# Optimization experiments

Hardware: AMD Instinct MI355X
Metric: run time of the kernel (lower is better)

Reference implementation:

```python
import jax, jax.numpy as jnp
import numpy as np

ALPHA = 1.0
BETA = 0.5

B, N, E = 4096, 4096, 16384


def setup_inputs() -> dict:
    key = jax.random.key(0)
    k1, k2, k3, k4, k5 = jax.random.split(key, 5)
    outputs = jax.random.normal(k1, (B, N), dtype=jnp.float32)
    targets = jax.random.uniform(k2, (B, N), dtype=jnp.float32)
    # per-node level weight (equivalent to node_levels dict -> level_weights lookup)
    level_w = jax.random.uniform(k3, (N,), dtype=jnp.float32)
    edge_src = jax.random.randint(k4, (E,), 0, N, dtype=jnp.int32)  # parent i
    edge_dst = jax.random.randint(k5, (E,), 0, N, dtype=jnp.int32)  # child  j
    return {"outputs": outputs, "targets": targets, "level_w": level_w,
            "edge_src": edge_src, "edge_dst": edge_dst}


def reference(outputs, targets, level_w, edge_src, edge_dst):
    # BCEWithLogits, reduction='none': softplus(x) - x*t (numerically stable)
    bce = jax.nn.softplus(outputs) - outputs * targets          # [B, N]
    weighted_bce = bce * level_w[None, :]                        # [B, N]

    probs = jax.nn.sigmoid(outputs)                              # [B, N]
    # for each edge (i=parent, j=child): consistency[:, j] += relu(p[:, j] - p[:, i])
    diff = jax.nn.relu(probs[:, edge_dst] - probs[:, edge_src])  # [B, E]
    consistency = jnp.zeros_like(probs).at[:, edge_dst].add(diff)  # [B, N]

    return ALPHA * weighted_bce.mean() + BETA * consistency.mean()
```

## Files before the change

kernel.cpp:

```cpp
#include <hip/hip_runtime.h>
#include <math.h>


#define ALPHA_C 1.0f
#define BETA_C  0.5f

constexpr int B = 4096;
constexpr int N = 4096;
constexpr int E = 16384;
constexpr int THREADS = 512;
constexpr int R = 4;

typedef _Float16 h4 __attribute__((ext_vector_type(4)));

__global__ __launch_bounds__(64) void init_out_kernel(float* out) {
    if (threadIdx.x == 0) out[0] = 0.0f;
}

__device__ __forceinline__ void fast_sig_sp(float x, float& p, float& sp) {
    float q = __expf(-fabsf(x));
    float d = 1.0f + q;
    float r = __builtin_amdgcn_rcpf(d);
    p  = (x >= 0.0f) ? r : q * r;
    sp = fmaxf(x, 0.0f) + __logf(d);
}

__global__ __launch_bounds__(THREADS, 8) void hier_loss_kernel(
    const float* __restrict__ outputs,
    const float* __restrict__ targets,
    const float* __restrict__ level_w,
    const int*   __restrict__ edge_src,
    const int*   __restrict__ edge_dst,
    float*       __restrict__ out)
{
    __shared__ h4 P[N];

    const int r0  = blockIdx.x * R;
    const int tid = threadIdx.x;

    const float4* out4 = (const float4*)outputs;
    const float4* tgt4 = (const float4*)targets;
    const float4* lw4  = (const float4*)level_w;

    float s1 = 0.0f;
#pragma unroll
    for (int j = 0; j < N / 4 / THREADS; ++j) {
        const int n4 = tid + j * THREADS;
        const float4 w = lw4[n4];
        const float wv[4] = {w.x, w.y, w.z, w.w};
        float4 xs[R], ts[R];
#pragma unroll
        for (int r = 0; r < R; ++r) {
            xs[r] = out4[(size_t)(r0 + r) * (N / 4) + n4];
            ts[r] = tgt4[(size_t)(r0 + r) * (N / 4) + n4];
        }
        h4 tmp[4];
#pragma unroll
        for (int r = 0; r < R; ++r) {
            const float xv[4] = {xs[r].x, xs[r].y, xs[r].z, xs[r].w};
            const float tv[4] = {ts[r].x, ts[r].y, ts[r].z, ts[r].w};
#pragma unroll
            for (int k = 0; k < 4; ++k) {
                float p, sp;
                fast_sig_sp(xv[k], p, sp);
                s1 = fmaf(wv[k], sp - xv[k] * tv[k], s1);
                tmp[k][r] = (_Float16)p;
            }
        }
#pragma unroll
        for (int k = 0; k < 4; ++k) P[4 * n4 + k] = tmp[k];
    }
    __syncthreads();

    h4 acc0 = {0, 0, 0, 0};
    h4 acc1 = {0, 0, 0, 0};
    const h4 zero = {0, 0, 0, 0};
    const int4* es4 = (const int4*)edge_src;
    const int4* ed4 = (const int4*)edge_dst;
#pragma unroll
    for (int j = 0; j < E / 4 / THREADS; ++j) {
        const int i = tid + j * THREADS;
        const int4 s = es4[i];
        const int4 d = ed4[i];
        h4 a0 = P[s.x], c0 = P[d.x];
        h4 a1 = P[s.y], c1 = P[d.y];
        h4 a2 = P[s.z], c2 = P[d.z];
        h4 a3 = P[s.w], c3 = P[d.w];
        acc0 += __builtin_elementwise_max(c0 - a0, zero);
        acc1 += __builtin_elementwise_max(c1 - a1, zero);
        acc0 += __builtin_elementwise_max(c2 - a2, zero);
        acc1 += __builtin_elementwise_max(c3 - a3, zero);
    }
    float s2 = 0.0f;
#pragma unroll
    for (int l = 0; l < 4; ++l) s2 += (float)acc0[l] + (float)acc1[l];

#pragma unroll
    for (int off = 32; off > 0; off >>= 1) {
        s1 += __shfl_down(s1, off, 64);
        s2 += __shfl_down(s2, off, 64);
    }
    __syncthreads();
    float* red = (float*)P;
    const int wave = tid >> 6;
    const int lane = tid & 63;
    if (lane == 0) { red[wave] = s1; red[8 + wave] = s2; }
    __syncthreads();
    if (tid == 0) {
        float a = 0.0f, c = 0.0f;
#pragma unroll
        for (int w = 0; w < 8; ++w) { a += red[w]; c += red[8 + w]; }
        const float inv = 1.0f / ((float)B * (float)N);
        atomicAdd(out, (ALPHA_C * a + BETA_C * c) * inv);
    }
}

extern "C" void kernel_launch(void* const* d_in, const int* in_sizes, int n_in,
                              void* d_out, int out_size, void* d_ws, size_t ws_size,
                              hipStream_t stream) {
    const float* outputs = (const float*)d_in[0];
    const float* targets = (const float*)d_in[1];
    const float* level_w = (const float*)d_in[2];
    const int*   edge_src = (const int*)d_in[3];
    const int*   edge_dst = (const int*)d_in[4];
    float* out = (float*)d_out;

    init_out_kernel<<<1, 64, 0, stream>>>(out);
    hier_loss_kernel<<<B / R, THREADS, 0, stream>>>(outputs, targets, level_w,
                                                    edge_src, edge_dst, out);
}
```

Baseline: 156.3 us.

## Make blocks persistent over row groups with double-buffered LDS and prefetch

The grid shrinks to 256 blocks of 1024 threads. Each block walks several 4-row groups and keeps its edge indices in registers, so they are loaded once per block rather than once per row group. Probabilities go into a double-buffered LDS array, and the next group's logits and targets are prefetched while the current group's edge gather runs. This cuts repeated edge-index traffic and overlaps global loads with the LDS gather phase. The cost is lower occupancy per CU and more register pressure.

Result: no change. 154.6 us, median of 2 (-1.1%).

```diff
diff --git a/kernel.cpp b/kernel.cpp
--- a/kernel.cpp
+++ b/kernel.cpp
@@ -8,8 +8,11 @@
 constexpr int B = 4096;
 constexpr int N = 4096;
 constexpr int E = 16384;
-constexpr int THREADS = 512;
+constexpr int THREADS = 1024;
 constexpr int R = 4;
+constexpr int GRID = 256;
+constexpr int GPB = (B / R) / GRID;
+constexpr int EJ = E / 4 / THREADS;
 
 typedef _Float16 h4 __attribute__((ext_vector_type(4)));
 
@@ -25,7 +28,7 @@
     sp = fmaxf(x, 0.0f) + __logf(d);
 }
 
-__global__ __launch_bounds__(THREADS, 8) void hier_loss_kernel(
+__global__ __launch_bounds__(THREADS, 4) void hier_loss_kernel(
     const float* __restrict__ outputs,
     const float* __restrict__ targets,
     const float* __restrict__ level_w,
@@ -33,27 +36,37 @@
     const int*   __restrict__ edge_dst,
     float*       __restrict__ out)
 {
-    __shared__ h4 P[N];
+    __shared__ h4 P[2][N];
 
-    const int r0  = blockIdx.x * R;
     const int tid = threadIdx.x;
+    const int g0  = blockIdx.x * GPB;
 
     const float4* out4 = (const float4*)outputs;
     const float4* tgt4 = (const float4*)targets;
     const float4* lw4  = (const float4*)level_w;
+    const int4*   es4  = (const int4*)edge_src;
+    const int4*   ed4  = (const int4*)edge_dst;
 
-    float s1 = 0.0f;
+    const float4 w = lw4[tid];
+    const float wv[4] = {w.x, w.y, w.z, w.w};
+
+    int4 se[EJ], de[EJ];
 #pragma unroll
-    for (int j = 0; j < N / 4 / THREADS; ++j) {
-        const int n4 = tid + j * THREADS;
-        const float4 w = lw4[n4];
-        const float wv[4] = {w.x, w.y, w.z, w.w};
-        float4 xs[R], ts[R];
+    for (int j = 0; j < EJ; ++j) {
+        se[j] = es4[tid + j * THREADS];
+        de[j] = ed4[tid + j * THREADS];
+    }
+
+    float s1 = 0.0f, s2 = 0.0f;
+    float4 xs[R], ts[R];
+
 #pragma unroll
-        for (int r = 0; r < R; ++r) {
-            xs[r] = out4[(size_t)(r0 + r) * (N / 4) + n4];
-            ts[r] = tgt4[(size_t)(r0 + r) * (N / 4) + n4];
-        }
+    for (int r = 0; r < R; ++r) {
+        const size_t row = (size_t)((g0 + 0) * R + r) * (N / 4) + tid;
+        xs[r] = out4[row];
+        ts[r] = tgt4[row];
+    }
+    {
         h4 tmp[4];
 #pragma unroll
         for (int r = 0; r < R; ++r) {
@@ -68,48 +81,75 @@
             }
         }
 #pragma unroll
-        for (int k = 0; k < 4; ++k) P[4 * n4 + k] = tmp[k];
+        for (int k = 0; k < 4; ++k) P[0][4 * tid + k] = tmp[k];
     }
     __syncthreads();
 
-    h4 acc0 = {0, 0, 0, 0};
-    h4 acc1 = {0, 0, 0, 0};
-    const h4 zero = {0, 0, 0, 0};
-    const int4* es4 = (const int4*)edge_src;
-    const int4* ed4 = (const int4*)edge_dst;
 #pragma unroll
-    for (int j = 0; j < E / 4 / THREADS; ++j) {
-        const int i = tid + j * THREADS;
-        const int4 s = es4[i];
-        const int4 d = ed4[i];
-        h4 a0 = P[s.x], c0 = P[d.x];
-        h4 a1 = P[s.y], c1 = P[d.y];
-        h4 a2 = P[s.z], c2 = P[d.z];
-        h4 a3 = P[s.w], c3 = P[d.w];
-        acc0 += __builtin_elementwise_max(c0 - a0, zero);
-        acc1 += __builtin_elementwise_max(c1 - a1, zero);
-        acc0 += __builtin_elementwise_max(c2 - a2, zero);
-        acc1 += __builtin_elementwise_max(c3 - a3, zero);
+    for (int kg = 0; kg < GPB; ++kg) {
+        if (kg + 1 < GPB) {
+#pragma unroll
+            for (int r = 0; r < R; ++r) {
+                const size_t row = (size_t)((g0 + kg + 1) * R + r) * (N / 4) + tid;
+                xs[r] = out4[row];
+                ts[r] = tgt4[row];
+            }
+        }
+
+        const h4* Pc = P[kg & 1];
+        h4 acc0 = {0, 0, 0, 0};
+        h4 acc1 = {0, 0, 0, 0};
+        const h4 zero = {0, 0, 0, 0};
+#pragma unroll
+        for (int j = 0; j < EJ; ++j) {
+            const int4 s = se[j];
+            const int4 d = de[j];
+            h4 a0 = Pc[s.x], c0 = Pc[d.x];
+            h4 a1 = Pc[s.y], c1 = Pc[d.y];
+            h4 a2 = Pc[s.z], c2 = Pc[d.z];
+            h4 a3 = Pc[s.w], c3 = Pc[d.w];
+            acc0 += __builtin_elementwise_max(c0 - a0, zero);
+            acc1 += __builtin_elementwise_max(c1 - a1, zero);
+            acc0 += __builtin_elementwise_max(c2 - a2, zero);
+            acc1 += __builtin_elementwise_max(c3 - a3, zero);
+        }
+#pragma unroll
+        for (int l = 0; l < 4; ++l) s2 += (float)acc0[l] + (float)acc1[l];
+
+        if (kg + 1 < GPB) {
+            h4 tmp[4];
+#pragma unroll
+            for (int r = 0; r < R; ++r) {
+                const float xv[4] = {xs[r].x, xs[r].y, xs[r].z, xs[r].w};
+                const float tv[4] = {ts[r].x, ts[r].y, ts[r].z, ts[r].w};
+#pragma unroll
+                for (int k = 0; k < 4; ++k) {
+                    float p, sp;
+                    fast_sig_sp(xv[k], p, sp);
+                    s1 = fmaf(wv[k], sp - xv[k] * tv[k], s1);
+                    tmp[k][r] = (_Float16)p;
+                }
+            }
+#pragma unroll
+            for (int k = 0; k < 4; ++k) P[(kg + 1) & 1][4 * tid + k] = tmp[k];
+        }
+        __syncthreads();
     }
-    float s2 = 0.0f;
-#pragma unroll
-    for (int l = 0; l < 4; ++l) s2 += (float)acc0[l] + (float)acc1[l];
 
 #pragma unroll
     for (int off = 32; off > 0; off >>= 1) {
         s1 += __shfl_down(s1, off, 64);
         s2 += __shfl_down(s2, off, 64);
     }
-    __syncthreads();
     float* red = (float*)P;
     const int wave = tid >> 6;
     const int lane = tid & 63;
-    if (lane == 0) { red[wave] = s1; red[8 + wave] = s2; }
+    if (lane == 0) { red[wave] = s1; red[16 + wave] = s2; }
     __syncthreads();
     if (tid == 0) {
         float a = 0.0f, c = 0.0f;
 #pragma unroll
-        for (int w = 0; w < 8; ++w) { a += red[w]; c += red[8 + w]; }
+        for (int v = 0; v < 16; ++v) { a += red[v]; c += red[16 + v]; }
         const float inv = 1.0f / ((float)B * (float)N);
         atomicAdd(out, (ALPHA_C * a + BETA_C * c) * inv);
     }
@@ -126,6 +166,6 @@
     float* out = (float*)d_out;
 
     init_out_kernel<<<1, 64, 0, stream>>>(out);
-    hier_loss_kernel<<<B / R, THREADS, 0, stream>>>(outputs, targets, level_w,
-                                                    edge_src, edge_dst, out);
+    hier_loss_kernel<<<GRID, THREADS, 0, stream>>>(outputs, targets, level_w,
+                                                   edge_src, edge_dst, out);
 }
```

## Split into elementwise sigmoid/BCE kernel and double-buffered edge kernel

Applied to the files above, without the earlier changes.

Splits the fused kernel in two. The first kernel computes BCE and writes fp16 sigmoid probabilities to a global workspace. The second kernel loads the edge indices into registers once, then processes four row-groups per block, streaming each group's probabilities into LDS with async global_load_lds double buffering. The goal is to amortise edge-index loads across row-groups and to overlap loading probabilities with the gather work. The cost is an extra 32 MB write and read through the workspace plus a second launch, and the old fused kernel is kept as a fallback.

After: 171.3 us. +9.6%, slower.

```diff
diff --git a/kernel.cpp b/kernel.cpp
--- a/kernel.cpp
+++ b/kernel.cpp
@@ -8,10 +8,10 @@
 constexpr int B = 4096;
 constexpr int N = 4096;
 constexpr int E = 16384;
-constexpr int THREADS = 512;
-constexpr int R = 4;
+constexpr size_t PG_BYTES = (size_t)B * N * 2;
 
 typedef _Float16 h4 __attribute__((ext_vector_type(4)));
+typedef _Float16 h8 __attribute__((ext_vector_type(8)));
 
 __global__ __launch_bounds__(64) void init_out_kernel(float* out) {
     if (threadIdx.x == 0) out[0] = 0.0f;
@@ -25,7 +25,154 @@
     sp = fmaxf(x, 0.0f) + __logf(d);
 }
 
-__global__ __launch_bounds__(THREADS, 8) void hier_loss_kernel(
+__global__ __launch_bounds__(512, 8) void sig_bce_kernel(
+    const float* __restrict__ outputs,
+    const float* __restrict__ targets,
+    const float* __restrict__ level_w,
+    h4*          __restrict__ Pg,
+    float*       __restrict__ out)
+{
+    const int tid  = threadIdx.x;
+    const int tile = blockIdx.x >> 1;
+    const int col4 = ((blockIdx.x & 1) << 9) + tid;
+
+    const float4* out4 = (const float4*)outputs;
+    const float4* tgt4 = (const float4*)targets;
+    const float4 w = ((const float4*)level_w)[col4];
+    const float wv[4] = {w.x, w.y, w.z, w.w};
+
+    float4 xs[4], ts[4];
+#pragma unroll
+    for (int r = 0; r < 4; ++r) {
+        const size_t idx = (size_t)(4 * tile + r) * (N / 4) + col4;
+        xs[r] = out4[idx];
+        ts[r] = tgt4[idx];
+    }
+
+    float s1 = 0.0f;
+    h4 tmp[4];
+#pragma unroll
+    for (int r = 0; r < 4; ++r) {
+        const float xv[4] = {xs[r].x, xs[r].y, xs[r].z, xs[r].w};
+        const float tv[4] = {ts[r].x, ts[r].y, ts[r].z, ts[r].w};
+#pragma unroll
+        for (int k = 0; k < 4; ++k) {
+            float p, sp;
+            fast_sig_sp(xv[k], p, sp);
+            s1 = fmaf(wv[k], sp - xv[k] * tv[k], s1);
+            tmp[k][r] = (_Float16)p;
+        }
+    }
+    h8 lo = __builtin_shufflevector(tmp[0], tmp[1], 0, 1, 2, 3, 4, 5, 6, 7);
+    h8 hi = __builtin_shufflevector(tmp[2], tmp[3], 0, 1, 2, 3, 4, 5, 6, 7);
+    h8* dst = (h8*)&Pg[(size_t)tile * N + 4 * col4];
+    dst[0] = lo;
+    dst[1] = hi;
+
+#pragma unroll
+    for (int off = 32; off > 0; off >>= 1) s1 += __shfl_down(s1, off, 64);
+    __shared__ float red[8];
+    const int wave = tid >> 6, lane = tid & 63;
+    if (lane == 0) red[wave] = s1;
+    __syncthreads();
+    if (tid == 0) {
+        float a = 0.0f;
+#pragma unroll
+        for (int v = 0; v < 8; ++v) a += red[v];
+        const float inv = 1.0f / ((float)B * (float)N);
+        atomicAdd(out, ALPHA_C * a * inv);
+    }
+}
+
+__global__ __launch_bounds__(1024, 4) void edge_kernel(
+    const h4* __restrict__ Pg,
+    const int* __restrict__ edge_src,
+    const int* __restrict__ edge_dst,
+    float*     __restrict__ out)
+{
+    __shared__ h4 Pl[2][N];
+
+    const int tid = threadIdx.x;
+    const int wv_ = tid >> 6;
+    const int ln  = tid & 63;
+    constexpr int EPT4 = E / 4 / 1024;
+
+    const int4* es4 = (const int4*)edge_src;
+    const int4* ed4 = (const int4*)edge_dst;
+
+    auto copy_grp = [&](int t, int bufi) {
+        const char* gbase = (const char*)&Pg[(size_t)t * N];
+#pragma unroll
+        for (int c = 0; c < 2; ++c) {
+            const int boff = (c * 16 + wv_) * 1024;
+            __builtin_amdgcn_global_load_lds(
+                (const __attribute__((address_space(1))) void*)(gbase + boff + ln * 16),
+                (__attribute__((address_space(3))) void*)((char*)&Pl[bufi][0] + boff),
+                16, 0, 0);
+        }
+    };
+
+    int4 se[EPT4], de[EPT4];
+#pragma unroll
+    for (int j = 0; j < EPT4; ++j) {
+        se[j] = es4[tid + j * 1024];
+        de[j] = ed4[tid + j * 1024];
+    }
+    copy_grp(blockIdx.x * 4 + 0, 0);
+    asm volatile("s_waitcnt vmcnt(0)" ::: "memory");
+    __builtin_amdgcn_s_barrier();
+
+    float s2 = 0.0f;
+#pragma unroll
+    for (int k = 0; k < 4; ++k) {
+        if (k + 1 < 4) copy_grp(blockIdx.x * 4 + k + 1, (k + 1) & 1);
+        __builtin_amdgcn_sched_barrier(0);
+
+        const h4* Pc = Pl[k & 1];
+        h4 acc0 = {0, 0, 0, 0};
+        h4 acc1 = {0, 0, 0, 0};
+        const h4 zero = {0, 0, 0, 0};
+#pragma unroll
+        for (int j = 0; j < EPT4; ++j) {
+            const int4 s = se[j];
+            const int4 d = de[j];
+            h4 a0 = Pc[s.x], c0 = Pc[d.x];
+            h4 a1 = Pc[s.y], c1 = Pc[d.y];
+            h4 a2 = Pc[s.z], c2 = Pc[d.z];
+            h4 a3 = Pc[s.w], c3 = Pc[d.w];
+            acc0 += __builtin_elementwise_max(c0 - a0, zero);
+            acc1 += __builtin_elementwise_max(c1 - a1, zero);
+            acc0 += __builtin_elementwise_max(c2 - a2, zero);
+            acc1 += __builtin_elementwise_max(c3 - a3, zero);
+        }
+#pragma unroll
+        for (int l = 0; l < 4; ++l) s2 += (float)acc0[l] + (float)acc1[l];
+
+        if (k + 1 < 4) {
+            asm volatile("s_waitcnt vmcnt(0)" ::: "memory");
+            __builtin_amdgcn_s_barrier();
+        }
+    }
+
+#pragma unroll
+    for (int off = 32; off > 0; off >>= 1) s2 += __shfl_down(s2, off, 64);
+    __syncthreads();
+    float* red = (float*)Pl;
+    if (ln == 0) red[wv_] = s2;
+    __syncthreads();
+    if (tid == 0) {
+        float c = 0.0f;
+#pragma unroll
+        for (int v = 0; v < 16; ++v) c += red[v];
+        const float inv = 1.0f / ((float)B * (float)N);
+        atomicAdd(out, BETA_C * c * inv);
+    }
+}
+
+constexpr int FTHREADS = 512;
+constexpr int FR = 4;
+
+__global__ __launch_bounds__(FTHREADS, 8) void hier_loss_fallback(
     const float* __restrict__ outputs,
     const float* __restrict__ targets,
     const float* __restrict__ level_w,
@@ -35,7 +182,7 @@
 {
     __shared__ h4 P[N];
 
-    const int r0  = blockIdx.x * R;
+    const int r0  = blockIdx.x * FR;
     const int tid = threadIdx.x;
 
     const float4* out4 = (const float4*)outputs;
@@ -44,19 +191,19 @@
 
     float s1 = 0.0f;
 #pragma unroll
-    for (int j = 0; j < N / 4 / THREADS; ++j) {
-        const int n4 = tid + j * THREADS;
+    for (int j = 0; j < N / 4 / FTHREADS; ++j) {
+        const int n4 = tid + j * FTHREADS;
         const float4 w = lw4[n4];
         const float wv[4] = {w.x, w.y, w.z, w.w};
-        float4 xs[R], ts[R];
-#pragma unroll
-        for (int r = 0; r < R; ++r) {
+        float4 xs[FR], ts[FR];
+#pragma unroll
+        for (int r = 0; r < FR; ++r) {
             xs[r] = out4[(size_t)(r0 + r) * (N / 4) + n4];
             ts[r] = tgt4[(size_t)(r0 + r) * (N / 4) + n4];
         }
         h4 tmp[4];
 #pragma unroll
-        for (int r = 0; r < R; ++r) {
+        for (int r = 0; r < FR; ++r) {
             const float xv[4] = {xs[r].x, xs[r].y, xs[r].z, xs[r].w};
             const float tv[4] = {ts[r].x, ts[r].y, ts[r].z, ts[r].w};
 #pragma unroll
@@ -78,8 +225,8 @@
     const int4* es4 = (const int4*)edge_src;
     const int4* ed4 = (const int4*)edge_dst;
 #pragma unroll
-    for (int j = 0; j < E / 4 / THREADS; ++j) {
-        const int i = tid + j * THREADS;
+    for (int j = 0; j < E / 4 / FTHREADS; ++j) {
+        const int i = tid + j * FTHREADS;
         const int4 s = es4[i];
         const int4 d = ed4[i];
         h4 a0 = P[s.x], c0 = P[d.x];
@@ -126,6 +273,12 @@
     float* out = (float*)d_out;
 
     init_out_kernel<<<1, 64, 0, stream>>>(out);
-    hier_loss_kernel<<<B / R, THREADS, 0, stream>>>(outputs, targets, level_w,
-                                                    edge_src, edge_dst, out);
-}
+    if (ws_size >= PG_BYTES && d_ws != nullptr) {
+        h4* Pg = (h4*)d_ws;
+        sig_bce_kernel<<<2048, 512, 0, stream>>>(outputs, targets, level_w, Pg, out);
+        edge_kernel<<<256, 1024, 0, stream>>>(Pg, edge_src, edge_dst, out);
+    } else {
+        hier_loss_fallback<<<B / FR, FTHREADS, 0, stream>>>(
+            outputs, targets, level_w, edge_src, edge_dst, out);
+    }
+}
```
